# Kernel tuning notes

Hardware: AMD Instinct MI355X
Metric: run time of the kernel (lower is better)

## Reference

```python
import jax, jax.numpy as jnp
import numpy as np

OUT_FEATURES = 14336
IN_FEATURES = 4096
BLOCK = 64

NF4_MAPPING = jnp.array([
    -1.0, -0.6961928009986877, -0.5250730514526367, -0.39491748809814453,
    -0.28444138169288635, -0.18477343022823334, -0.09105003625154495, 0.0,
    0.07958029955625534, 0.16093020141124725, 0.24611230194568634,
    0.33791524171829224, 0.44070982933044434, 0.5626170039176941,
    0.7229568362236023, 1.0], dtype=jnp.float32)


def setup_inputs() -> dict:
    key = jax.random.key(0)
    k1, k2, k3, k4, k5 = jax.random.split(key, 5)
    x = jax.random.normal(k1, (8192, IN_FEATURES), dtype=jnp.float32)
    w_packed = jax.random.randint(k2, (OUT_FEATURES * IN_FEATURES // 2,), 0, 256, dtype=jnp.int32)
    w_absmax = jax.random.uniform(k3, (OUT_FEATURES * IN_FEATURES // BLOCK,), dtype=jnp.float32)
    b_packed = jax.random.randint(k4, (OUT_FEATURES // 2,), 0, 256, dtype=jnp.int32)
    b_absmax = jax.random.uniform(k5, (OUT_FEATURES // BLOCK,), dtype=jnp.float32)
    return {"x": x, "w_packed": w_packed, "w_absmax": w_absmax,
            "b_packed": b_packed, "b_absmax": b_absmax}


def _nf4_dequantize(packed, absmax, shape):
    # Each byte holds two 4-bit codes: (hi*16 + lo); unpack in (hi, lo) order
    # exactly like torch.stack([w // 16, w % 16], dim=1).view(-1).
    codes = jnp.stack([packed // 16, packed % 16], axis=-1).reshape(-1)
    vals = NF4_MAPPING[codes]                       # [N] dequantized in [-1, 1]
    blocks = vals.reshape(-1, BLOCK) * absmax.reshape(-1, 1)  # per-block rescale
    return blocks.reshape(shape)


def reference(x, w_packed, w_absmax, b_packed, b_absmax):
    weight = _nf4_dequantize(w_packed, w_absmax, (OUT_FEATURES, IN_FEATURES))
    bias = _nf4_dequantize(b_packed, b_absmax, (OUT_FEATURES,))
    return jnp.matmul(x, weight.T) + bias
```

## Files before the change

kernel.cpp:

```cpp
#include <hip/hip_runtime.h>

typedef unsigned short u16;
typedef signed char s8;
typedef __attribute__((ext_vector_type(4))) float f32x4;
typedef __attribute__((ext_vector_type(4))) int i32x4;

#define M_ROWS 8192
#define N_OUT  14336
#define K_IN   4096
#define NTILE  64

__constant__ float NF4_TAB[16] = {
    -1.0f, -0.6961928009986877f, -0.5250730514526367f, -0.39491748809814453f,
    -0.28444138169288635f, -0.18477343022823334f, -0.09105003625154495f, 0.0f,
    0.07958029955625534f, 0.16093020141124725f, 0.24611230194568634f,
    0.33791524171829224f, 0.44070982933044434f, 0.5626170039176941f,
    0.7229568362236023f, 1.0f};

static __device__ __forceinline__ void async_load16(const void* g, void* l) {
  __builtin_amdgcn_global_load_lds(
      (const __attribute__((address_space(1))) void*)g,
      (__attribute__((address_space(3))) void*)l, 16, 0, 0);
}

__global__ __launch_bounds__(256) void quant_w_kernel(
    const int* __restrict__ wp, const float* __restrict__ wa,
    s8* __restrict__ wout, float* __restrict__ sn) {
  const int n = blockIdx.x;
  const int t = threadIdx.x, lane = t & 63, wid = t >> 6;
  const i32x4 p0 = __builtin_nontemporal_load(
      reinterpret_cast<const i32x4*>(wp) + (size_t)n * 512 + 2 * t);
  const i32x4 p1 = __builtin_nontemporal_load(
      reinterpret_cast<const i32x4*>(wp) + (size_t)n * 512 + 2 * t + 1);
  const float am = wa[n * 64 + (t >> 2)];

  float v[16];
  int pv[8] = {p0.x, p0.y, p0.z, p0.w, p1.x, p1.y, p1.z, p1.w};
  float mx = 0.0f;
#pragma unroll
  for (int i = 0; i < 8; ++i) {
    v[2 * i]     = NF4_TAB[(pv[i] >> 4) & 15];
    v[2 * i + 1] = NF4_TAB[pv[i] & 15];
  }
#pragma unroll
  for (int i = 0; i < 16; ++i) mx = fmaxf(mx, fabsf(v[i]));
  mx *= am;
#pragma unroll
  for (int off = 32; off; off >>= 1) mx = fmaxf(mx, __shfl_xor(mx, off));
  __shared__ float red[4];
  if (lane == 0) red[wid] = mx;
  __syncthreads();
  const float colmax = fmaxf(fmaxf(red[0], red[1]), fmaxf(red[2], red[3]));
  const float inv = colmax > 0.0f ? (127.0f * am) / colmax : 0.0f;

  union { s8 c[16]; i32x4 q; } o;
#pragma unroll
  for (int i = 0; i < 16; ++i) o.c[i] = (s8)(int)rintf(v[i] * inv);
  reinterpret_cast<i32x4*>(wout)[(size_t)n * 256 + t] = o.q;
  if (t == 0) sn[n] = colmax * (1.0f / 127.0f);
}

__global__ __launch_bounds__(256) void quant_x_kernel(
    const float* __restrict__ x, s8* __restrict__ xi8,
    float* __restrict__ sxr) {
  const int row = blockIdx.x;
  const int tid = threadIdx.x, lane = tid & 63, wid = tid >> 6;
  const float4* xr = reinterpret_cast<const float4*>(x + (size_t)row * 4096);
  float4 v[4];
  float mx = 0.0f;
#pragma unroll
  for (int i = 0; i < 4; ++i) {
    v[i] = xr[tid * 4 + i];
    mx = fmaxf(mx, fmaxf(fmaxf(fabsf(v[i].x), fabsf(v[i].y)),
                         fmaxf(fabsf(v[i].z), fabsf(v[i].w))));
  }
#pragma unroll
  for (int off = 32; off; off >>= 1) mx = fmaxf(mx, __shfl_xor(mx, off));
  __shared__ float red[4];
  if (lane == 0) red[wid] = mx;
  __syncthreads();
  mx = fmaxf(fmaxf(red[0], red[1]), fmaxf(red[2], red[3]));
  float rs = mx > 0.0f ? 127.0f / mx : 0.0f;
  union { s8 c[16]; i32x4 q; } o;
#pragma unroll
  for (int i = 0; i < 4; ++i) {
    o.c[4 * i + 0] = (s8)(int)rintf(v[i].x * rs);
    o.c[4 * i + 1] = (s8)(int)rintf(v[i].y * rs);
    o.c[4 * i + 2] = (s8)(int)rintf(v[i].z * rs);
    o.c[4 * i + 3] = (s8)(int)rintf(v[i].w * rs);
  }
  reinterpret_cast<i32x4*>(xi8 + (size_t)row * 4096)[tid] = o.q;
  if (tid == 0) sxr[row] = mx * (1.0f / 127.0f);
}

__global__ __launch_bounds__(512, 2) void gemm_nf4_i8(
    const s8* __restrict__ A,
    const s8* __restrict__ B,
    float* __restrict__ C, const int* __restrict__ bp,
    const float* __restrict__ ba, const float* __restrict__ sn,
    const float* __restrict__ sxr) {
  constexpr int K = K_IN, N = N_OUT;
  extern __shared__ char smem[];
  char* sA = smem;
  char* sB = smem + 32768;

  const int tid = threadIdx.x;
  const int w = tid >> 6, lane = tid & 63;
  const int r = lane & 15, kq = lane >> 4;
  const int wr = w >> 2, wc = w & 3;

  int bid = blockIdx.x;
  int cpx = gridDim.x >> 3;
  int wg = (bid & 7) * cpx + (bid >> 3);
  int grp = wg / 448;
  int rem = wg - grp * 448;
  int nt = rem >> 3;
  int mt = grp * 8 + (rem & 7);
  const size_t m0 = (size_t)mt * 256, n0 = (size_t)nt * 256;

  const s8* gA = A + m0 * K;
  const s8* gB = B + n0 * K;

  const int cswz = ((kq ^ ((r >> 1) & 3)) << 4);
  const int cg16 = (((lane & 3) ^ ((lane >> 3) & 3)) << 4);
  const int rl = lane >> 2;

  const s8* stA0 = gA + (size_t)(w * 16 + rl) * K + cg16;
  const s8* stA1 = gA + (size_t)(128 + w * 16 + rl) * K + cg16;
  const s8* stB0 = gB + (size_t)(w * 16 + rl) * K + cg16;
  const s8* stB1 = gB + (size_t)(128 + w * 16 + rl) * K + cg16;

  i32x4 acc[8][4] = {};
  i32x4 aF[4], bF[4];

#define BAR() __builtin_amdgcn_s_barrier()
#define VM(n) asm volatile("s_waitcnt vmcnt(" #n ")" ::: "memory")

#define STAGE_AB(P, s) do {                                                   \
    async_load16(stA0 + (size_t)(s) * 64, sA + (P) * 16384 + w * 1024);       \
    async_load16(stA1 + (size_t)(s) * 64, sA + (P) * 16384 + 8192 + w * 1024);\
    async_load16(stB0 + (size_t)(s) * 64, sB + (P) * 16384 + w * 1024);       \
    async_load16(stB1 + (size_t)(s) * 64, sB + (P) * 16384 + 8192 + w * 1024);\
  } while (0)

#define READ_A(P, mq) do {                                                   \
    const char* pa_ = sA + (P) * 16384 + (wr * 128 + (mq) * 64 + r) * 64;    \
    _Pragma("unroll")                                                        \
    for (int m_ = 0; m_ < 4; ++m_)                                           \
      aF[m_] = *(const i32x4*)(pa_ + m_ * 1024 + cswz);                      \
  } while (0)

#define READ_B(P, nq) do {                                                   \
    const char* pb_ = sB + (P) * 16384 + (wc * 64 + (nq) * 32 + r) * 64;     \
    _Pragma("unroll")                                                        \
    for (int n_ = 0; n_ < 2; ++n_)                                           \
      bF[(nq) * 2 + n_] = *(const i32x4*)(pb_ + n_ * 1024 + cswz);           \
  } while (0)

#define MFMA_Q(mq, nq) do {                                                  \
    __builtin_amdgcn_s_setprio(1);                                           \
    _Pragma("unroll")                                                        \
    for (int m_ = 0; m_ < 4; ++m_)                                           \
      _Pragma("unroll")                                                      \
      for (int n_ = 0; n_ < 2; ++n_)                                         \
        acc[(mq) * 4 + m_][(nq) * 2 + n_] =                                  \
            __builtin_amdgcn_mfma_i32_16x16x64_i8(                           \
                aF[m_], bF[(nq) * 2 + n_],                                   \
                acc[(mq) * 4 + m_][(nq) * 2 + n_], 0, 0, 0);                 \
    __builtin_amdgcn_s_setprio(0);                                           \
  } while (0)

#define BODY(s, P, DO_STAGE, DO_VMBAR) do {                                  \
    READ_A(P, 0); READ_B(P, 0);                                              \
    if (DO_STAGE) STAGE_AB((P) ^ 1, (s) + 1);                                \
    MFMA_Q(0, 0);                                                            \
    READ_B(P, 1); MFMA_Q(0, 1);                                              \
    READ_A(P, 1); MFMA_Q(1, 0); MFMA_Q(1, 1);                                \
    if (DO_VMBAR) { VM(0); BAR(); }                                          \
  } while (0)

  STAGE_AB(0, 0);
  VM(0); BAR();

  for (int s = 0; s < NTILE - 2; s += 2) {
    BODY(s, 0, 1, 1);
    BODY(s + 1, 1, 1, 1);
  }
  BODY(NTILE - 2, 0, 1, 1);
  BODY(NTILE - 1, 1, 0, 0);

  float bias[4], snv[4];
#pragma unroll
  for (int ni = 0; ni < 4; ++ni) {
    int col = (int)n0 + wc * 64 + ni * 16 + r;
    int byte = bp[col >> 1];
    int code = (col & 1) ? (byte & 15) : ((byte >> 4) & 15);
    bias[ni] = NF4_TAB[code] * ba[col >> 6];
    snv[ni] = sn[col];
  }
#pragma unroll
  for (int mi = 0; mi < 8; ++mi) {
    size_t row0 = m0 + wr * 128 + mi * 16 + kq * 4;
    const f32x4 sxv = *reinterpret_cast<const f32x4*>(sxr + row0);
#pragma unroll
    for (int ni = 0; ni < 4; ++ni) {
      size_t col = n0 + wc * 64 + ni * 16 + r;
#pragma unroll
      for (int j = 0; j < 4; ++j)
        C[(row0 + j) * N + col] =
            (float)acc[mi][ni][j] * (snv[ni] * sxv[j]) + bias[ni];
    }
  }
#undef BODY
#undef MFMA_Q
#undef READ_B
#undef READ_A
#undef STAGE_AB
#undef VM
#undef BAR
}

extern "C" void kernel_launch(void* const* d_in, const int* in_sizes, int n_in,
                              void* d_out, int out_size, void* d_ws,
                              size_t ws_size, hipStream_t stream) {
  const float* x  = (const float*)d_in[0];
  const int* wp   = (const int*)d_in[1];
  const float* wa = (const float*)d_in[2];
  const int* bp   = (const int*)d_in[3];
  const float* ba = (const float*)d_in[4];
  float* out = (float*)d_out;

  s8* Wi8 = (s8*)d_ws;
  s8* Xi8 = Wi8 + (size_t)N_OUT * K_IN;
  float* sn  = (float*)(Xi8 + (size_t)M_ROWS * K_IN);
  float* sxr = sn + N_OUT;

  quant_w_kernel<<<N_OUT, 256, 0, stream>>>(wp, wa, Wi8, sn);
  quant_x_kernel<<<M_ROWS, 256, 0, stream>>>(x, Xi8, sxr);

  hipFuncSetAttribute(reinterpret_cast<const void*>(gemm_nf4_i8),
                      hipFuncAttributeMaxDynamicSharedMemorySize, 65536);
  gemm_nf4_i8<<<1792, 512, 65536, stream>>>(Xi8, Wi8, out, bp, ba, sn, sxr);
}
```

Baseline: 619.7 us.

## Shrink GEMM block tile to 256x128 and raise occupancy target

The int8 GEMM block tile drops from 256x256 to 256x128. Warps are rearranged 4x2, so each warp owns a 64x64 sub-tile with 16 accumulators instead of 32, and B fragments are loaded inline inside the MFMA loop. Shared memory falls to 48 KiB and the grid doubles, with launch bounds now asking for 4 blocks per CU to hide latency better. In exchange, each A tile is reloaded twice as often, reuse per loaded byte drops, and the tighter register budget may force spills.

After: 615.5 us. Within noise of the previous version (-0.7%).

```diff
diff --git a/kernel.cpp b/kernel.cpp
--- a/kernel.cpp
+++ b/kernel.cpp
@@ -93,7 +93,7 @@
   if (tid == 0) sxr[row] = mx * (1.0f / 127.0f);
 }
 
-__global__ __launch_bounds__(512, 2) void gemm_nf4_i8(
+__global__ __launch_bounds__(512, 4) void gemm_nf4_i8(
     const s8* __restrict__ A,
     const s8* __restrict__ B,
     float* __restrict__ C, const int* __restrict__ bp,
@@ -107,16 +107,16 @@
   const int tid = threadIdx.x;
   const int w = tid >> 6, lane = tid & 63;
   const int r = lane & 15, kq = lane >> 4;
-  const int wr = w >> 2, wc = w & 3;
+  const int wr = w >> 1, wc = w & 1;
 
   int bid = blockIdx.x;
   int cpx = gridDim.x >> 3;
   int wg = (bid & 7) * cpx + (bid >> 3);
-  int grp = wg / 448;
-  int rem = wg - grp * 448;
+  int grp = wg / 896;
+  int rem = wg - grp * 896;
   int nt = rem >> 3;
   int mt = grp * 8 + (rem & 7);
-  const size_t m0 = (size_t)mt * 256, n0 = (size_t)nt * 256;
+  const size_t m0 = (size_t)mt * 256, n0 = (size_t)nt * 128;
 
   const s8* gA = A + m0 * K;
   const s8* gB = B + n0 * K;
@@ -128,10 +128,9 @@
   const s8* stA0 = gA + (size_t)(w * 16 + rl) * K + cg16;
   const s8* stA1 = gA + (size_t)(128 + w * 16 + rl) * K + cg16;
   const s8* stB0 = gB + (size_t)(w * 16 + rl) * K + cg16;
-  const s8* stB1 = gB + (size_t)(128 + w * 16 + rl) * K + cg16;
-
-  i32x4 acc[8][4] = {};
-  i32x4 aF[4], bF[4];
+
+  i32x4 acc[4][4] = {};
+  i32x4 aF[4];
 
 #define BAR() __builtin_amdgcn_s_barrier()
 #define VM(n) asm volatile("s_waitcnt vmcnt(" #n ")" ::: "memory")
@@ -139,43 +138,34 @@
 #define STAGE_AB(P, s) do {                                                   \
     async_load16(stA0 + (size_t)(s) * 64, sA + (P) * 16384 + w * 1024);       \
     async_load16(stA1 + (size_t)(s) * 64, sA + (P) * 16384 + 8192 + w * 1024);\
-    async_load16(stB0 + (size_t)(s) * 64, sB + (P) * 16384 + w * 1024);       \
-    async_load16(stB1 + (size_t)(s) * 64, sB + (P) * 16384 + 8192 + w * 1024);\
-  } while (0)
-
-#define READ_A(P, mq) do {                                                   \
-    const char* pa_ = sA + (P) * 16384 + (wr * 128 + (mq) * 64 + r) * 64;    \
+    async_load16(stB0 + (size_t)(s) * 64, sB + (P) * 8192 + w * 1024);        \
+  } while (0)
+
+#define READ_A(P) do {                                                       \
+    const char* pa_ = sA + (P) * 16384 + (wr * 64 + r) * 64;                 \
     _Pragma("unroll")                                                        \
     for (int m_ = 0; m_ < 4; ++m_)                                           \
       aF[m_] = *(const i32x4*)(pa_ + m_ * 1024 + cswz);                      \
   } while (0)
 
-#define READ_B(P, nq) do {                                                   \
-    const char* pb_ = sB + (P) * 16384 + (wc * 64 + (nq) * 32 + r) * 64;     \
-    _Pragma("unroll")                                                        \
-    for (int n_ = 0; n_ < 2; ++n_)                                           \
-      bF[(nq) * 2 + n_] = *(const i32x4*)(pb_ + n_ * 1024 + cswz);           \
-  } while (0)
-
-#define MFMA_Q(mq, nq) do {                                                  \
+#define MFMA_ALL(P) do {                                                     \
+    const char* pb_ = sB + (P) * 8192 + (wc * 64 + r) * 64;                  \
     __builtin_amdgcn_s_setprio(1);                                           \
     _Pragma("unroll")                                                        \
-    for (int m_ = 0; m_ < 4; ++m_)                                           \
+    for (int n_ = 0; n_ < 4; ++n_) {                                         \
+      i32x4 bF_ = *(const i32x4*)(pb_ + n_ * 1024 + cswz);                   \
       _Pragma("unroll")                                                      \
-      for (int n_ = 0; n_ < 2; ++n_)                                         \
-        acc[(mq) * 4 + m_][(nq) * 2 + n_] =                                  \
-            __builtin_amdgcn_mfma_i32_16x16x64_i8(                           \
-                aF[m_], bF[(nq) * 2 + n_],                                   \
-                acc[(mq) * 4 + m_][(nq) * 2 + n_], 0, 0, 0);                 \
+      for (int m_ = 0; m_ < 4; ++m_)                                         \
+        acc[m_][n_] = __builtin_amdgcn_mfma_i32_16x16x64_i8(                 \
+            aF[m_], bF_, acc[m_][n_], 0, 0, 0);                              \
+    }                                                                        \
     __builtin_amdgcn_s_setprio(0);                                           \
   } while (0)
 
 #define BODY(s, P, DO_STAGE, DO_VMBAR) do {                                  \
-    READ_A(P, 0); READ_B(P, 0);                                              \
+    READ_A(P);                                                               \
     if (DO_STAGE) STAGE_AB((P) ^ 1, (s) + 1);                                \
-    MFMA_Q(0, 0);                                                            \
-    READ_B(P, 1); MFMA_Q(0, 1);                                              \
-    READ_A(P, 1); MFMA_Q(1, 0); MFMA_Q(1, 1);                                \
+    MFMA_ALL(P);                                                             \
     if (DO_VMBAR) { VM(0); BAR(); }                                          \
   } while (0)
 
@@ -199,8 +189,8 @@
     snv[ni] = sn[col];
   }
 #pragma unroll
-  for (int mi = 0; mi < 8; ++mi) {
-    size_t row0 = m0 + wr * 128 + mi * 16 + kq * 4;
+  for (int mi = 0; mi < 4; ++mi) {
+    size_t row0 = m0 + wr * 64 + mi * 16 + kq * 4;
     const f32x4 sxv = *reinterpret_cast<const f32x4*>(sxr + row0);
 #pragma unroll
     for (int ni = 0; ni < 4; ++ni) {
@@ -212,8 +202,7 @@
     }
   }
 #undef BODY
-#undef MFMA_Q
-#undef READ_B
+#undef MFMA_ALL
 #undef READ_A
 #undef STAGE_AB
 #undef VM
@@ -239,6 +228,6 @@
   quant_x_kernel<<<M_ROWS, 256, 0, stream>>>(x, Xi8, sxr);
 
   hipFuncSetAttribute(reinterpret_cast<const void*>(gemm_nf4_i8),
-                      hipFuncAttributeMaxDynamicSharedMemorySize, 65536);
-  gemm_nf4_i8<<<1792, 512, 65536, stream>>>(Xi8, Wi8, out, bp, ba, sn, sxr);
-}
+                      hipFuncAttributeMaxDynamicSharedMemorySize, 49152);
+  gemm_nf4_i8<<<3584, 512, 49152, stream>>>(Xi8, Wi8, out, bp, ba, sn, sxr);
+}
```
